# Optimization experiments

Hardware: AMD Instinct MI355X
Metric: run time of the kernel (lower is better)

Reference implementation:

```python
import jax, jax.numpy as jnp
import numpy as np

HEADS = 16
DIM_HEAD = 64
SCALE = DIM_HEAD ** -0.5


def setup_inputs() -> dict:
    key = jax.random.key(0)
    ks = jax.random.split(key, 7)
    b, n, m, d = 2, 2048, 2048, 1024
    inner = HEADS * DIM_HEAD  # 1024
    patch_embed = jax.random.normal(ks[0], (b, n, d), dtype=jnp.float32)
    pixel_embed = jax.random.normal(ks[1], (b, m, d), dtype=jnp.float32)
    s = 1.0 / np.sqrt(d)
    Wq = jax.random.normal(ks[2], (d, inner), dtype=jnp.float32) * s
    Wk = jax.random.normal(ks[3], (d, inner), dtype=jnp.float32) * s
    Wv = jax.random.normal(ks[4], (d, inner), dtype=jnp.float32) * s
    Wo = jax.random.normal(ks[5], (inner, d), dtype=jnp.float32) * (1.0 / np.sqrt(inner))
    bo = jax.random.normal(ks[6], (d,), dtype=jnp.float32) * 0.01
    return {"patch_embed": patch_embed, "pixel_embed": pixel_embed,
            "Wq": Wq, "Wk": Wk, "Wv": Wv, "Wo": Wo, "bo": bo}


def reference(patch_embed, pixel_embed, Wq, Wk, Wv, Wo, bo):
    b, n, _ = patch_embed.shape
    h, dh = HEADS, DIM_HEAD
    # projections
    q = patch_embed @ Wq  # [b, n, h*dh]
    k = pixel_embed @ Wk  # [b, m, h*dh]
    v = pixel_embed @ Wv  # [b, m, h*dh]
    # split heads: [b, seq, h, dh]
    q = q.reshape(b, n, h, dh)
    k = k.reshape(b, -1, h, dh)
    v = v.reshape(b, -1, h, dh)
    sim = jnp.einsum('bihd,bjhd->bhij', q, k) * SCALE  # [b, h, n, m]
    attn = jax.nn.softmax(sim, axis=-1)
    out = jnp.einsum('bhij,bjhd->bihd', attn, v)  # [b, n, h, dh]
    out = out.reshape(b, n, h * dh)
    return out @ Wo + bo  # [b, n, query_dim]
```

## Files before the change

kernel.cpp:

```cpp
#include <hip/hip_runtime.h>

#define SEQ 2048
#define DMODEL 1024
#define HEADS 16
#define DH 64
#define QSCALE 0.180336880f

typedef __attribute__((ext_vector_type(8))) short short8;
typedef __attribute__((ext_vector_type(4))) float f32x4;

__device__ __forceinline__ ushort f2bf(float x) {
  union { float f; unsigned u; } v; v.f = x;
  return (ushort)((v.u + 0x7fffu + ((v.u >> 16) & 1u)) >> 16);
}

__device__ __forceinline__ void gld16(const ushort* g, ushort* l) {
  __builtin_amdgcn_global_load_lds(
      (const __attribute__((address_space(1))) unsigned int*)g,
      (__attribute__((address_space(3))) unsigned int*)l, 16, 0, 0);
}

__device__ __forceinline__ size_t qk_idx(int bh, int s, int d) {
  return ((((size_t)bh * (SEQ / 16) + (s >> 4)) * 2 + (d >> 5)) * 64 +
          ((d >> 3) & 3) * 16 + (s & 15)) * 8 + (d & 7);
}
__device__ __forceinline__ size_t v_idx(int bh, int s, int d) {
  return ((((size_t)bh * 4 + (d >> 4)) * (SEQ / 32) + (s >> 5)) * 64 +
          ((s >> 3) & 3) * 16 + (d & 15)) * 8 + (s & 7);
}

__global__ __launch_bounds__(256) void prologue(
    const float* __restrict__ patch, const float* __restrict__ pixel,
    const float* __restrict__ W0, const float* __restrict__ W1,
    const float* __restrict__ W2, const float* __restrict__ W3,
    ushort* __restrict__ pb, ushort* __restrict__ xb,
    ushort* __restrict__ O0, ushort* __restrict__ O1,
    ushort* __restrict__ O2, ushort* __restrict__ O3) {
  const int z = blockIdx.z;
  const int tx = threadIdx.x, ty = threadIdx.y;
  if (z < 2) {
    const float4* in = (const float4*)(z ? pixel : patch);
    ushort4* out = (ushort4*)(z ? xb : pb);
    const int base = (blockIdx.y * 32 + blockIdx.x) * 256 + ty * 32 + tx;
#pragma unroll
    for (int rep = 0; rep < 4; ++rep) {
      const int i = base + rep * 262144;
      float4 f = in[i];
      out[i] = make_ushort4(f2bf(f.x), f2bf(f.y), f2bf(f.z), f2bf(f.w));
    }
    return;
  }
  __shared__ float tile[32][33];
  const int zz = z - 2;
  const float* in = zz == 0 ? W0 : zz == 1 ? W1 : zz == 2 ? W2 : W3;
  ushort* out = zz == 0 ? O0 : zz == 1 ? O1 : zz == 2 ? O2 : O3;
  const float scale = zz == 0 ? QSCALE : 1.0f;
  const int n0 = blockIdx.x * 32, k0 = blockIdx.y * 32;
#pragma unroll
  for (int i = 0; i < 4; ++i)
    tile[ty + i * 8][tx] = in[(size_t)(k0 + ty + i * 8) * DMODEL + n0 + tx];
  __syncthreads();
#pragma unroll
  for (int i = 0; i < 4; ++i)
    out[(size_t)(n0 + ty + i * 8) * DMODEL + k0 + tx] =
        f2bf(tile[tx][ty + i * 8] * scale);
}

__global__ __launch_bounds__(256) void mfma_gemm_qkv(
    const ushort* __restrict__ pb, const ushort* __restrict__ xb,
    const ushort* __restrict__ wqt, const ushort* __restrict__ wkt,
    const ushort* __restrict__ wvt, ushort* __restrict__ qws,
    ushort* __restrict__ kws, ushort* __restrict__ vws) {
  __shared__ __align__(16) ushort As[128 * 64];
  __shared__ __align__(16) ushort Bs[128 * 64];
  const int z = blockIdx.z;
  const ushort* A = (z == 0) ? pb : xb;
  const ushort* Bt = (z == 0) ? wqt : (z == 1) ? wkt : wvt;

  const int t = threadIdx.x;
  const int w = t >> 6, lane = t & 63, ln = lane & 15, q = lane >> 4;
  const int wm = w & 1, wn = w >> 1;
  const int row0 = blockIdx.y * 128, col0 = blockIdx.x * 128;
  const int sw = ln & 7;

  f32x4 acc[4][4];
#pragma unroll
  for (int i = 0; i < 4; ++i)
#pragma unroll
    for (int j = 0; j < 4; ++j) acc[i][j] = (f32x4){0.f, 0.f, 0.f, 0.f};

  for (int k0 = 0; k0 < DMODEL; k0 += 64) {
    __syncthreads();
#pragma unroll
    for (int rep = 0; rep < 4; ++rep) {
      const int u0 = rep * 256 + w * 64;
      const int u = u0 + lane;
      const int r = u >> 3, gl = (u & 7) ^ (r & 7);
      gld16(&A[(size_t)(row0 + r) * DMODEL + k0 + gl * 8], &As[u0 * 8]);
      gld16(&Bt[(size_t)(col0 + r) * DMODEL + k0 + gl * 8], &Bs[u0 * 8]);
    }
    __syncthreads();
#pragma unroll
    for (int ks = 0; ks < 2; ++ks) {
      short8 af[4], bf[4];
#pragma unroll
      for (int rt = 0; rt < 4; ++rt)
        af[rt] = *(const short8*)&As[(wm * 64 + rt * 16 + ln) * 64 +
                                     (((ks * 4 + q) ^ sw) * 8)];
#pragma unroll
      for (int ct = 0; ct < 4; ++ct)
        bf[ct] = *(const short8*)&Bs[(wn * 64 + ct * 16 + ln) * 64 +
                                     (((ks * 4 + q) ^ sw) * 8)];
#pragma unroll
      for (int rt = 0; rt < 4; ++rt)
#pragma unroll
        for (int ct = 0; ct < 4; ++ct)
          acc[rt][ct] = __builtin_amdgcn_mfma_f32_16x16x32_bf16(af[rt], bf[ct],
                                                                acc[rt][ct], 0, 0, 0);
    }
  }

  if (z < 2) {
    ushort* dst = z == 0 ? qws : kws;
#pragma unroll
    for (int rt = 0; rt < 4; ++rt)
#pragma unroll
      for (int ct = 0; ct < 4; ++ct) {
        const int c = col0 + wn * 64 + ct * 16 + ln;
        const int h = c >> 6, d = c & 63;
#pragma unroll
        for (int reg = 0; reg < 4; ++reg) {
          const int r = row0 + wm * 64 + rt * 16 + q * 4 + reg;
          const int b = r >> 11, s = r & (SEQ - 1);
          dst[qk_idx(b * HEADS + h, s, d)] = f2bf(acc[rt][ct][reg]);
        }
      }
  } else {
#pragma unroll
    for (int rt = 0; rt < 4; ++rt)
#pragma unroll
      for (int ct = 0; ct < 4; ++ct) {
        const int c = col0 + wn * 64 + ct * 16 + ln;
        const int h = c >> 6, d = c & 63;
        const int r0 = row0 + wm * 64 + rt * 16 + q * 4;
        const int b = r0 >> 11, s0 = r0 & (SEQ - 1);
        ushort4 u4 = make_ushort4(f2bf(acc[rt][ct][0]), f2bf(acc[rt][ct][1]),
                                  f2bf(acc[rt][ct][2]), f2bf(acc[rt][ct][3]));
        *(ushort4*)&vws[v_idx(b * HEADS + h, s0, d)] = u4;
      }
  }
}

__global__ __launch_bounds__(256, 4) void flash_mfma(
    const ushort* __restrict__ Qg, const ushort* __restrict__ Kg,
    const ushort* __restrict__ Vg, float* __restrict__ PO0,
    float* __restrict__ PO1, float* __restrict__ L0, float* __restrict__ L1) {
  __shared__ __align__(16) ushort Kst[8 * 512];
  __shared__ __align__(16) ushort Vst[8 * 512];
  __shared__ __align__(16) ushort Ps[128 * 72];

  const int t = threadIdx.x;
  const int w = t >> 6, lane = t & 63, ln = lane & 15, q = lane >> 4;
  const int qt = blockIdx.x;
  const int bh = blockIdx.y;
  const int seg = blockIdx.z;

  float* __restrict__ PO = seg ? PO1 : PO0;
  float* __restrict__ Lb = seg ? L1 : L0;

  const ushort* qg = Qg + (size_t)bh * SEQ * DH;
  const ushort* kg = Kg + (size_t)bh * SEQ * DH;
  const ushort* vg = Vg + (size_t)bh * DH * SEQ;

  short8 qf[2][2];
#pragma unroll
  for (int rt = 0; rt < 2; ++rt)
#pragma unroll
    for (int ks = 0; ks < 2; ++ks)
      qf[rt][ks] = *(const short8*)
          &qg[(((size_t)(qt * 8 + w * 2 + rt) * 2 + ks) * 64 + lane) * 8];

  float l_i[2][4];
  f32x4 acc_o[2][4];
#pragma unroll
  for (int rt = 0; rt < 2; ++rt)
#pragma unroll
    for (int reg = 0; reg < 4; ++reg) l_i[rt][reg] = 0.f;
#pragma unroll
  for (int rt = 0; rt < 2; ++rt)
#pragma unroll
    for (int nt = 0; nt < 4; ++nt) acc_o[rt][nt] = (f32x4){0.f, 0.f, 0.f, 0.f};

  for (int kt = seg * 16; kt < seg * 16 + 16; ++kt) {
    __syncthreads();
#pragma unroll
    for (int i = 0; i < 4; ++i) {
      const int f = w * 4 + i;
      if (f < 8) {
        gld16(&kg[((size_t)(kt * 8 + f)) * 512 + lane * 8], &Kst[f * 512]);
      } else {
        const int f2 = f - 8, nt = f2 >> 1, ks2 = f2 & 1;
        gld16(&vg[((size_t)(nt * (SEQ / 32) + kt * 2 + ks2)) * 512 + lane * 8],
              &Vst[f2 * 512]);
      }
    }
    __syncthreads();

    f32x4 accs[2][4];
#pragma unroll
    for (int rt = 0; rt < 2; ++rt)
#pragma unroll
      for (int ct = 0; ct < 4; ++ct) accs[rt][ct] = (f32x4){0.f, 0.f, 0.f, 0.f};
#pragma unroll
    for (int ks = 0; ks < 2; ++ks)
#pragma unroll
      for (int ct = 0; ct < 4; ++ct) {
        const short8 bf = *(const short8*)&Kst[(ct * 2 + ks) * 512 + lane * 8];
#pragma unroll
        for (int rt = 0; rt < 2; ++rt)
          accs[rt][ct] = __builtin_amdgcn_mfma_f32_16x16x32_bf16(
              qf[rt][ks], bf, accs[rt][ct], 0, 0, 0);
      }

#pragma unroll
    for (int rt = 0; rt < 2; ++rt)
#pragma unroll
      for (int ct = 0; ct < 4; ++ct)
#pragma unroll
        for (int reg = 0; reg < 4; ++reg) {
          const float p = __builtin_amdgcn_exp2f(accs[rt][ct][reg]);
          l_i[rt][reg] += p;
          union { float f; unsigned u; } v; v.f = p;
          Ps[(w * 32 + rt * 16 + q * 4 + reg) * 72 + ct * 16 + ln] =
              (ushort)((v.u + 0x8000u) >> 16);
        }

#pragma unroll
    for (int ks2 = 0; ks2 < 2; ++ks2) {
      short8 pa[2];
#pragma unroll
      for (int rt = 0; rt < 2; ++rt)
        pa[rt] = *(const short8*)&Ps[(w * 32 + rt * 16 + ln) * 72 +
                                     ks2 * 32 + q * 8];
#pragma unroll
      for (int nt = 0; nt < 4; ++nt) {
        const short8 bv = *(const short8*)&Vst[(nt * 2 + ks2) * 512 + lane * 8];
#pragma unroll
        for (int rt = 0; rt < 2; ++rt)
          acc_o[rt][nt] = __builtin_amdgcn_mfma_f32_16x16x32_bf16(
              pa[rt], bv, acc_o[rt][nt], 0, 0, 0);
      }
    }
  }

#pragma unroll
  for (int rt = 0; rt < 2; ++rt)
#pragma unroll
    for (int reg = 0; reg < 4; ++reg) {
      float l = l_i[rt][reg];
      l += __shfl_xor(l, 1, 16);
      l += __shfl_xor(l, 2, 16);
      l += __shfl_xor(l, 4, 16);
      l += __shfl_xor(l, 8, 16);
      const int s = qt * 128 + w * 32 + rt * 16 + q * 4 + reg;
      if (ln == 0) Lb[bh * SEQ + s] = l;
#pragma unroll
      for (int nt = 0; nt < 4; ++nt)
        PO[((size_t)bh * SEQ + s) * DH + nt * 16 + ln] = acc_o[rt][nt][reg];
    }
}

__global__ __launch_bounds__(256) void merge_reduce(
    const float4* __restrict__ PO0, const float4* __restrict__ PO1,
    const float* __restrict__ L0, const float* __restrict__ L1,
    ushort* __restrict__ aws) {
  const int i = blockIdx.x * 256 + threadIdx.x;
  const int row = i >> 4, d4 = i & 15;
  const int bh = row >> 11, s = row & (SEQ - 1);
  const int b = bh >> 4, h = bh & 15;
  const float4 a = PO0[i];
  const float4 c = PO1[i];
  const float inv = 1.0f / (L0[row] + L1[row]);
  ushort4 u = make_ushort4(f2bf((a.x + c.x) * inv), f2bf((a.y + c.y) * inv),
                           f2bf((a.z + c.z) * inv), f2bf((a.w + c.w) * inv));
  *(ushort4*)&aws[((size_t)b * SEQ + s) * DMODEL + h * DH + d4 * 4] = u;
}

__global__ __launch_bounds__(256) void mfma_gemm_out(const ushort* __restrict__ A,
                                                     const ushort* __restrict__ Bt,
                                                     const float* __restrict__ bias,
                                                     float* __restrict__ dst) {
  __shared__ __align__(16) ushort As[64 * 64];
  __shared__ __align__(16) ushort Bs[128 * 64];
  const int t = threadIdx.x;
  const int w = t >> 6, lane = t & 63, ln = lane & 15, q = lane >> 4;
  const int wm = w & 1, wn = w >> 1;
  const int row0 = blockIdx.y * 64, col0 = blockIdx.x * 128;
  const int sw = ln & 7;

  f32x4 acc[2][4];
#pragma unroll
  for (int i = 0; i < 2; ++i)
#pragma unroll
    for (int j = 0; j < 4; ++j) acc[i][j] = (f32x4){0.f, 0.f, 0.f, 0.f};

  for (int k0 = 0; k0 < DMODEL; k0 += 64) {
    __syncthreads();
#pragma unroll
    for (int rep = 0; rep < 2; ++rep) {
      const int u0 = rep * 256 + w * 64;
      const int u = u0 + lane;
      const int r = u >> 3, gl = (u & 7) ^ (r & 7);
      gld16(&A[(size_t)(row0 + r) * DMODEL + k0 + gl * 8], &As[u0 * 8]);
    }
#pragma unroll
    for (int rep = 0; rep < 4; ++rep) {
      const int u0 = rep * 256 + w * 64;
      const int u = u0 + lane;
      const int r = u >> 3, gl = (u & 7) ^ (r & 7);
      gld16(&Bt[(size_t)(col0 + r) * DMODEL + k0 + gl * 8], &Bs[u0 * 8]);
    }
    __syncthreads();
#pragma unroll
    for (int ks = 0; ks < 2; ++ks) {
      short8 af[2], bf[4];
#pragma unroll
      for (int rt = 0; rt < 2; ++rt)
        af[rt] = *(const short8*)&As[(wm * 32 + rt * 16 + ln) * 64 +
                                     (((ks * 4 + q) ^ sw) * 8)];
#pragma unroll
      for (int ct = 0; ct < 4; ++ct)
        bf[ct] = *(const short8*)&Bs[(wn * 64 + ct * 16 + ln) * 64 +
                                     (((ks * 4 + q) ^ sw) * 8)];
#pragma unroll
      for (int rt = 0; rt < 2; ++rt)
#pragma unroll
        for (int ct = 0; ct < 4; ++ct)
          acc[rt][ct] = __builtin_amdgcn_mfma_f32_16x16x32_bf16(af[rt], bf[ct],
                                                                acc[rt][ct], 0, 0, 0);
    }
  }

#pragma unroll
  for (int rt = 0; rt < 2; ++rt)
#pragma unroll
    for (int ct = 0; ct < 4; ++ct) {
      const int c = col0 + wn * 64 + ct * 16 + ln;
      const float bi = bias[c];
#pragma unroll
      for (int reg = 0; reg < 4; ++reg) {
        const int r = row0 + wm * 32 + rt * 16 + q * 4 + reg;
        dst[(size_t)r * DMODEL + c] = acc[rt][ct][reg] + bi;
      }
    }
}

extern "C" void kernel_launch(void* const* d_in, const int* in_sizes, int n_in,
                              void* d_out, int out_size, void* d_ws,
                              size_t ws_size, hipStream_t stream) {
  const float* patch = (const float*)d_in[0];
  const float* pixel = (const float*)d_in[1];
  const float* Wq = (const float*)d_in[2];
  const float* Wk = (const float*)d_in[3];
  const float* Wv = (const float*)d_in[4];
  const float* Wo = (const float*)d_in[5];
  const float* bo = (const float*)d_in[6];
  float* out = (float*)d_out;

  const size_t E = (size_t)2 * SEQ * DMODEL;
  const size_t W = (size_t)DMODEL * DMODEL;
  ushort* pb  = (ushort*)d_ws;
  ushort* xb  = pb + E;
  ushort* wqt = xb + E;
  ushort* wkt = wqt + W;
  ushort* wvt = wkt + W;
  ushort* wot = wvt + W;
  ushort* qws = wot + W;
  ushort* kws = qws + E;
  ushort* vws = kws + E;
  ushort* aws = vws + E;

  float* PO0 = (float*)pb;
  float* PO1 = out;
  float* L0 = (float*)wqt;
  float* L1 = L0 + 32 * SEQ;

  prologue<<<dim3(32, 32, 6), dim3(32, 8), 0, stream>>>(
      patch, pixel, Wq, Wk, Wv, Wo, pb, xb, wqt, wkt, wvt, wot);
  mfma_gemm_qkv<<<dim3(8, 32, 3), 256, 0, stream>>>(pb, xb, wqt, wkt, wvt,
                                                    qws, kws, vws);
  flash_mfma<<<dim3(16, 32, 2), 256, 0, stream>>>(qws, kws, vws, PO0, PO1, L0, L1);
  merge_reduce<<<dim3((32 * SEQ * DH / 4) / 256), 256, 0, stream>>>(
      (const float4*)PO0, (const float4*)PO1, L0, L1, aws);
  mfma_gemm_out<<<dim3(8, 64), 256, 0, stream>>>(aws, wot, bo, out);
}
```

Measured before the change: 207.8 us.

## Drop split-KV attention, double-buffer K/V loads, fuse normalization into flash kernel

The flash attention kernel no longer splits the KV sequence into two segments. Each block now walks all 32 KV tiles, with K/V tiles double-buffered in shared memory so the next tile's global-to-LDS load overlaps the current tile's MFMA work, and one barrier per iteration instead of two. Row sums are normalized in-kernel and bf16 output is written directly in the layout the output GEMM expects, which removes the merge_reduce launch and the fp32 partial-output round trip through memory. The trade-offs are half as many blocks (512 instead of 1024), twice as much LDS per block, and a launch-bounds occupancy hint lowered from 4 to 3. The grid order also changes to put bh on x.

```diff
diff --git a/kernel.cpp b/kernel.cpp
--- a/kernel.cpp
+++ b/kernel.cpp
@@ -151,22 +151,17 @@
   }
 }
 
-__global__ __launch_bounds__(256, 4) void flash_mfma(
+__global__ __launch_bounds__(256, 3) void flash_mfma(
     const ushort* __restrict__ Qg, const ushort* __restrict__ Kg,
-    const ushort* __restrict__ Vg, float* __restrict__ PO0,
-    float* __restrict__ PO1, float* __restrict__ L0, float* __restrict__ L1) {
-  __shared__ __align__(16) ushort Kst[8 * 512];
-  __shared__ __align__(16) ushort Vst[8 * 512];
+    const ushort* __restrict__ Vg, ushort* __restrict__ Og) {
+  __shared__ __align__(16) ushort Kst[2][8 * 512];
+  __shared__ __align__(16) ushort Vst[2][8 * 512];
   __shared__ __align__(16) ushort Ps[128 * 72];
 
   const int t = threadIdx.x;
   const int w = t >> 6, lane = t & 63, ln = lane & 15, q = lane >> 4;
-  const int qt = blockIdx.x;
-  const int bh = blockIdx.y;
-  const int seg = blockIdx.z;
-
-  float* __restrict__ PO = seg ? PO1 : PO0;
-  float* __restrict__ Lb = seg ? L1 : L0;
+  const int bh = blockIdx.x;
+  const int qt = blockIdx.y;
 
   const ushort* qg = Qg + (size_t)bh * SEQ * DH;
   const ushort* kg = Kg + (size_t)bh * SEQ * DH;
@@ -191,20 +186,37 @@
 #pragma unroll
     for (int nt = 0; nt < 4; ++nt) acc_o[rt][nt] = (f32x4){0.f, 0.f, 0.f, 0.f};
 
-  for (int kt = seg * 16; kt < seg * 16 + 16; ++kt) {
-    __syncthreads();
-#pragma unroll
-    for (int i = 0; i < 4; ++i) {
-      const int f = w * 4 + i;
-      if (f < 8) {
-        gld16(&kg[((size_t)(kt * 8 + f)) * 512 + lane * 8], &Kst[f * 512]);
-      } else {
-        const int f2 = f - 8, nt = f2 >> 1, ks2 = f2 & 1;
-        gld16(&vg[((size_t)(nt * (SEQ / 32) + kt * 2 + ks2)) * 512 + lane * 8],
-              &Vst[f2 * 512]);
-      }
-    }
-    __syncthreads();
+#pragma unroll
+  for (int i = 0; i < 4; ++i) {
+    const int f = w * 4 + i;
+    if (f < 8) {
+      gld16(&kg[(size_t)(0 * 8 + f) * 512 + lane * 8], &Kst[0][f * 512]);
+    } else {
+      const int f2 = f - 8, nt = f2 >> 1, ks2 = f2 & 1;
+      gld16(&vg[(size_t)(nt * (SEQ / 32) + 0 * 2 + ks2) * 512 + lane * 8],
+            &Vst[0][f2 * 512]);
+    }
+  }
+  __syncthreads();
+
+  for (int kt = 0; kt < SEQ / 64; ++kt) {
+    const int cur = kt & 1;
+    if (kt + 1 < SEQ / 64) {
+      const int nxt = cur ^ 1;
+#pragma unroll
+      for (int i = 0; i < 4; ++i) {
+        const int f = w * 4 + i;
+        if (f < 8) {
+          gld16(&kg[(size_t)((kt + 1) * 8 + f) * 512 + lane * 8],
+                &Kst[nxt][f * 512]);
+        } else {
+          const int f2 = f - 8, nt = f2 >> 1, ks2 = f2 & 1;
+          gld16(&vg[(size_t)(nt * (SEQ / 32) + (kt + 1) * 2 + ks2) * 512 +
+                    lane * 8],
+                &Vst[nxt][f2 * 512]);
+        }
+      }
+    }
 
     f32x4 accs[2][4];
 #pragma unroll
@@ -215,7 +227,7 @@
     for (int ks = 0; ks < 2; ++ks)
 #pragma unroll
       for (int ct = 0; ct < 4; ++ct) {
-        const short8 bf = *(const short8*)&Kst[(ct * 2 + ks) * 512 + lane * 8];
+        const short8 bf = *(const short8*)&Kst[cur][(ct * 2 + ks) * 512 + lane * 8];
 #pragma unroll
         for (int rt = 0; rt < 2; ++rt)
           accs[rt][ct] = __builtin_amdgcn_mfma_f32_16x16x32_bf16(
@@ -244,15 +256,18 @@
                                      ks2 * 32 + q * 8];
 #pragma unroll
       for (int nt = 0; nt < 4; ++nt) {
-        const short8 bv = *(const short8*)&Vst[(nt * 2 + ks2) * 512 + lane * 8];
+        const short8 bv = *(const short8*)&Vst[cur][(nt * 2 + ks2) * 512 + lane * 8];
 #pragma unroll
         for (int rt = 0; rt < 2; ++rt)
           acc_o[rt][nt] = __builtin_amdgcn_mfma_f32_16x16x32_bf16(
               pa[rt], bv, acc_o[rt][nt], 0, 0, 0);
       }
     }
-  }
-
+
+    __syncthreads();
+  }
+
+  const int b = bh >> 4, h = bh & 15;
 #pragma unroll
   for (int rt = 0; rt < 2; ++rt)
 #pragma unroll
@@ -262,28 +277,13 @@
       l += __shfl_xor(l, 2, 16);
       l += __shfl_xor(l, 4, 16);
       l += __shfl_xor(l, 8, 16);
+      const float inv = 1.0f / l;
       const int s = qt * 128 + w * 32 + rt * 16 + q * 4 + reg;
-      if (ln == 0) Lb[bh * SEQ + s] = l;
 #pragma unroll
       for (int nt = 0; nt < 4; ++nt)
-        PO[((size_t)bh * SEQ + s) * DH + nt * 16 + ln] = acc_o[rt][nt][reg];
-    }
-}
-
-__global__ __launch_bounds__(256) void merge_reduce(
-    const float4* __restrict__ PO0, const float4* __restrict__ PO1,
-    const float* __restrict__ L0, const float* __restrict__ L1,
-    ushort* __restrict__ aws) {
-  const int i = blockIdx.x * 256 + threadIdx.x;
-  const int row = i >> 4, d4 = i & 15;
-  const int bh = row >> 11, s = row & (SEQ - 1);
-  const int b = bh >> 4, h = bh & 15;
-  const float4 a = PO0[i];
-  const float4 c = PO1[i];
-  const float inv = 1.0f / (L0[row] + L1[row]);
-  ushort4 u = make_ushort4(f2bf((a.x + c.x) * inv), f2bf((a.y + c.y) * inv),
-                           f2bf((a.z + c.z) * inv), f2bf((a.w + c.w) * inv));
-  *(ushort4*)&aws[((size_t)b * SEQ + s) * DMODEL + h * DH + d4 * 4] = u;
+        Og[(size_t)(b * SEQ + s) * DMODEL + h * DH + nt * 16 + ln] =
+            f2bf(acc_o[rt][nt][reg] * inv);
+    }
 }
 
 __global__ __launch_bounds__(256) void mfma_gemm_out(const ushort* __restrict__ A,
@@ -380,17 +380,10 @@
   ushort* vws = kws + E;
   ushort* aws = vws + E;
 
-  float* PO0 = (float*)pb;
-  float* PO1 = out;
-  float* L0 = (float*)wqt;
-  float* L1 = L0 + 32 * SEQ;
-
   prologue<<<dim3(32, 32, 6), dim3(32, 8), 0, stream>>>(
       patch, pixel, Wq, Wk, Wv, Wo, pb, xb, wqt, wkt, wvt, wot);
   mfma_gemm_qkv<<<dim3(8, 32, 3), 256, 0, stream>>>(pb, xb, wqt, wkt, wvt,
                                                     qws, kws, vws);
-  flash_mfma<<<dim3(16, 32, 2), 256, 0, stream>>>(qws, kws, vws, PO0, PO1, L0, L1);
-  merge_reduce<<<dim3((32 * SEQ * DH / 4) / 256), 256, 0, stream>>>(
-      (const float4*)PO0, (const float4*)PO1, L0, L1, aws);
+  flash_mfma<<<dim3(32, 16), 256, 0, stream>>>(qws, kws, vws, aws);
   mfma_gemm_out<<<dim3(8, 64), 256, 0, stream>>>(aws, wot, bo, out);
 }
```

Result: faster. 195.9 us (-5.7%).
